# Kernel optimization log

Measured on AMD Instinct MI355X. Metric: run time of the kernel, lower is better.

## Reference

```python
import jax, jax.numpy as jnp
import numpy as np

N_NODES = 100000
N_EDGES = 3200000
IN_F, HID, OUT_F = 128, 3, 4


def setup_inputs() -> dict:
    key = jax.random.key(0)
    k1, k2, k3, k4, k5, k6 = jax.random.split(key, 6)
    x = jax.random.normal(k1, (N_NODES, IN_F), dtype=jnp.float32)
    edge_index = jax.random.randint(k2, (2, N_EDGES), 0, N_NODES, dtype=jnp.int64)
    # GCNConv weight (glorot) + bias, Linear(3,4) weight + bias
    W = jax.random.normal(k3, (IN_F, HID), dtype=jnp.float32) * (1.0 / np.sqrt(IN_F))
    b = jnp.zeros((HID,), dtype=jnp.float32)
    Wout = jax.random.normal(k4, (HID, OUT_F), dtype=jnp.float32) * (1.0 / np.sqrt(HID))
    bout = jax.random.normal(k5, (OUT_F,), dtype=jnp.float32) * 0.01
    return {"x": x, "edge_index": edge_index, "W": W, "b": b, "Wout": Wout, "bout": bout}


def reference(x, edge_index, W, b, Wout, bout):
    N = x.shape[0]
    # add self loops (PyG GCNConv default: add_self_loops=True)
    loop = jnp.arange(N, dtype=edge_index.dtype)
    row = jnp.concatenate([edge_index[0], loop])  # source nodes
    col = jnp.concatenate([edge_index[1], loop])  # destination nodes
    # linear transform first (cheaper: 128 -> 3)
    xw = x @ W  # [N, 3]
    # symmetric degree normalization: deg computed on destination index
    deg = jax.ops.segment_sum(jnp.ones_like(col, dtype=x.dtype), col, num_segments=N)
    dinv = jnp.where(deg > 0, jax.lax.rsqrt(deg), 0.0)
    norm = dinv[row] * dinv[col]  # [E+N]
    # gather source features, scale, scatter-add to destinations
    msg = xw[row] * norm[:, None]  # [E+N, 3]
    agg = jax.ops.segment_sum(msg, col, num_segments=N)  # [N, 3]
    h = jax.nn.relu(agg + b)
    z = h @ Wout + bout
    return (h, z)
```

## Files before the change

### kernel.cpp

```cpp
#include <hip/hip_runtime.h>
#include <hip/hip_fp16.h>

#define N_NODES 100000
#define N_EDGES 3200000
#define IN_F    128
#define HID     3
#define OUT_F   4

#define BSHIFT  7
#define BSIZE   128
#define NBUCK   ((N_NODES + BSIZE - 1) / BSIZE)
#define NBLKA   512
#define EPB     ((N_EDGES + NBLKA - 1) / NBLKA)
#define NH      (NBUCK * NBLKA)

#define SCAN_ITEMS 16
#define SCAN_BLOCK 256
#define SCAN_PER_BLOCK (SCAN_ITEMS * SCAN_BLOCK)
#define NS1 ((NH + SCAN_PER_BLOCK - 1) / SCAN_PER_BLOCK)

#define NREP    4
#define RSTRIDE 392
#define CSTRIDE 136

typedef float f32x4 __attribute__((ext_vector_type(4)));


__global__ void xw_kernel(const float* __restrict__ x,
                          const float* __restrict__ W,
                          float* __restrict__ xw) {
    int wave = threadIdx.x >> 6;
    int lane = threadIdx.x & 63;
    int half = lane >> 5;
    int l    = lane & 31;
    int node = blockIdx.x * 8 + wave * 2 + half;
    if (node >= N_NODES) return;

    f32x4 xv = __builtin_nontemporal_load(
        reinterpret_cast<const f32x4*>(x + (size_t)node * IN_F + l * 4));
    const float* w = W + l * 4 * HID;
    float s0 = xv.x * w[0] + xv.y * w[3] + xv.z * w[6] + xv.w * w[9];
    float s1 = xv.x * w[1] + xv.y * w[4] + xv.z * w[7] + xv.w * w[10];
    float s2 = xv.x * w[2] + xv.y * w[5] + xv.z * w[8] + xv.w * w[11];
    #pragma unroll
    for (int off = 16; off > 0; off >>= 1) {
        s0 += __shfl_down(s0, off, 32);
        s1 += __shfl_down(s1, off, 32);
        s2 += __shfl_down(s2, off, 32);
    }
    if (l == 0) {
        xw[node * 3 + 0] = s0;
        xw[node * 3 + 1] = s1;
        xw[node * 3 + 2] = s2;
    }
}

__global__ __launch_bounds__(512) void histA_kernel(const int* __restrict__ col,
                                                    int* __restrict__ histG) {
    __shared__ int hist[NBUCK];
    int tid = threadIdx.x, blk = blockIdx.x;
    for (int i = tid; i < NBUCK; i += 512) hist[i] = 0;
    __syncthreads();
    int start = blk * EPB, end = min(start + EPB, N_EDGES);
    for (int e = start + tid; e < end; e += 512)
        atomicAdd(&hist[__builtin_nontemporal_load(&col[e]) >> BSHIFT], 1);
    __syncthreads();
    for (int i = tid; i < NBUCK; i += 512)
        histG[i * NBLKA + blk] = hist[i];
}

__global__ void scan1_kernel(int* __restrict__ data, int* __restrict__ bsum) {
    __shared__ int s[SCAN_BLOCK];
    int tid = threadIdx.x;
    int base = blockIdx.x * SCAN_PER_BLOCK + tid * SCAN_ITEMS;
    int v[SCAN_ITEMS];
    int tsum = 0;
    #pragma unroll
    for (int j = 0; j < SCAN_ITEMS; ++j) {
        v[j] = (base + j < NH) ? data[base + j] : 0;
        tsum += v[j];
    }
    s[tid] = tsum;
    __syncthreads();
    for (int off = 1; off < SCAN_BLOCK; off <<= 1) {
        int t = (tid >= off) ? s[tid - off] : 0;
        __syncthreads();
        s[tid] += t;
        __syncthreads();
    }
    int run = s[tid] - tsum;
    #pragma unroll
    for (int j = 0; j < SCAN_ITEMS; ++j) {
        int t = v[j];
        if (base + j < NH) data[base + j] = run;
        run += t;
    }
    if (tid == SCAN_BLOCK - 1) bsum[blockIdx.x] = s[SCAN_BLOCK - 1];
}

__global__ void scan2_kernel(int* __restrict__ bsum) {
    __shared__ int s[SCAN_BLOCK];
    int tid = threadIdx.x;
    int v = (tid < NS1) ? bsum[tid] : 0;
    s[tid] = v;
    __syncthreads();
    for (int off = 1; off < SCAN_BLOCK; off <<= 1) {
        int t = (tid >= off) ? s[tid - off] : 0;
        __syncthreads();
        s[tid] += t;
        __syncthreads();
    }
    if (tid < NS1) bsum[tid] = s[tid] - v;
}

__global__ void scan3_kernel(int* __restrict__ data, const int* __restrict__ bsum) {
    int i = blockIdx.x * blockDim.x + threadIdx.x;
    if (i < NH) data[i] += bsum[i / SCAN_PER_BLOCK];
}

__global__ __launch_bounds__(512) void fillB_kernel(const int* __restrict__ row,
                                                    const int* __restrict__ col,
                                                    const int* __restrict__ histG,
                                                    int* __restrict__ packed) {
    __shared__ int offs[NBUCK];
    int tid = threadIdx.x, blk = blockIdx.x;
    for (int i = tid; i < NBUCK; i += 512) offs[i] = histG[i * NBLKA + blk];
    __syncthreads();
    int start = blk * EPB, end = min(start + EPB, N_EDGES);
    for (int e = start + tid; e < end; e += 512) {
        int c = __builtin_nontemporal_load(&col[e]);
        int r = __builtin_nontemporal_load(&row[e]);
        int b = c >> BSHIFT;
        int pos = atomicAdd(&offs[b], 1);
        packed[pos] = (r << BSHIFT) | (c & (BSIZE - 1));
    }
}

__global__ __launch_bounds__(512, 8) void degC_kernel(const int* __restrict__ histG,
                                                      const int* __restrict__ packed,
                                                      const float* __restrict__ xw,
                                                      uint2* __restrict__ tab) {
    __shared__ int cnt[NREP * CSTRIDE];
    int tid = threadIdx.x, b = blockIdx.x;
    int rep = tid & (NREP - 1);
    for (int i = tid; i < NREP * CSTRIDE; i += 512) cnt[i] = 0;
    __syncthreads();
    int start = histG[b * NBLKA];
    int end   = (b + 1 < NBUCK) ? histG[(b + 1) * NBLKA] : N_EDGES;
    int len   = end - start;
    int nfull = len & ~(4 * 512 - 1);
    for (int off = tid; off < nfull; off += 2048) {
        int p0 = __builtin_nontemporal_load(&packed[start + off]);
        int p1 = __builtin_nontemporal_load(&packed[start + off + 512]);
        int p2 = __builtin_nontemporal_load(&packed[start + off + 1024]);
        int p3 = __builtin_nontemporal_load(&packed[start + off + 1536]);
        atomicAdd(&cnt[rep * CSTRIDE + (p0 & (BSIZE - 1))], 1);
        atomicAdd(&cnt[rep * CSTRIDE + (p1 & (BSIZE - 1))], 1);
        atomicAdd(&cnt[rep * CSTRIDE + (p2 & (BSIZE - 1))], 1);
        atomicAdd(&cnt[rep * CSTRIDE + (p3 & (BSIZE - 1))], 1);
    }
    for (int off = nfull + tid; off < len; off += 512)
        atomicAdd(&cnt[rep * CSTRIDE + (__builtin_nontemporal_load(&packed[start + off]) & (BSIZE - 1))], 1);
    __syncthreads();
    if (tid < BSIZE) {
        int node = b * BSIZE + tid;
        if (node < N_NODES) {
            int c = cnt[0 * CSTRIDE + tid] + cnt[1 * CSTRIDE + tid]
                  + cnt[2 * CSTRIDE + tid] + cnt[3 * CSTRIDE + tid];
            float d = rsqrtf((float)(c + 1));
            __half2 lo = __floats2half2_rn(xw[node * 3 + 0] * d, xw[node * 3 + 1] * d);
            __half2 hi = __floats2half2_rn(xw[node * 3 + 2] * d, d);
            uint2 u;
            u.x = *reinterpret_cast<unsigned int*>(&lo);
            u.y = *reinterpret_cast<unsigned int*>(&hi);
            tab[node] = u;
        }
    }
}

__device__ inline void unpack4(uint2 u, float& a, float& b, float& c, float& d) {
    __half2 lo = *reinterpret_cast<__half2*>(&u.x);
    __half2 hi = *reinterpret_cast<__half2*>(&u.y);
    float2 f0 = __half22float2(lo);
    float2 f1 = __half22float2(hi);
    a = f0.x; b = f0.y; c = f1.x; d = f1.y;
}

__global__ __launch_bounds__(512, 8) void aggC_kernel(const int* __restrict__ histG,
                                                      const int* __restrict__ packed,
                                                      const uint2* __restrict__ tab,
                                                      const float* __restrict__ bb,
                                                      const float* __restrict__ Wout,
                                                      const float* __restrict__ bout,
                                                      float* __restrict__ out) {
    __shared__ float acc[NREP * RSTRIDE];
    int tid = threadIdx.x, b = blockIdx.x;
    int rep = tid & (NREP - 1);
    float* myacc = acc + rep * RSTRIDE;
    for (int i = tid; i < NREP * RSTRIDE; i += 512) acc[i] = 0.f;
    __syncthreads();
    int start = histG[b * NBLKA];
    int end   = (b + 1 < NBUCK) ? histG[(b + 1) * NBLKA] : N_EDGES;
    int len   = end - start;
    int nfull = len & ~(4 * 512 - 1);
    for (int off = tid; off < nfull; off += 2048) {
        int p0 = __builtin_nontemporal_load(&packed[start + off]);
        int p1 = __builtin_nontemporal_load(&packed[start + off + 512]);
        int p2 = __builtin_nontemporal_load(&packed[start + off + 1024]);
        int p3 = __builtin_nontemporal_load(&packed[start + off + 1536]);
        uint2 u0 = tab[p0 >> BSHIFT];
        uint2 u1 = tab[p1 >> BSHIFT];
        uint2 u2 = tab[p2 >> BSHIFT];
        uint2 u3 = tab[p3 >> BSHIFT];
        float a0, b0, c0, d0, a1, b1, c1, d1, a2, b2, c2, d2, a3, b3, c3, d3;
        unpack4(u0, a0, b0, c0, d0);
        unpack4(u1, a1, b1, c1, d1);
        unpack4(u2, a2, b2, c2, d2);
        unpack4(u3, a3, b3, c3, d3);
        int i0 = (p0 & (BSIZE - 1)) * 3, i1 = (p1 & (BSIZE - 1)) * 3;
        int i2 = (p2 & (BSIZE - 1)) * 3, i3 = (p3 & (BSIZE - 1)) * 3;
        atomicAdd(&myacc[i0 + 0], a0); atomicAdd(&myacc[i0 + 1], b0); atomicAdd(&myacc[i0 + 2], c0);
        atomicAdd(&myacc[i1 + 0], a1); atomicAdd(&myacc[i1 + 1], b1); atomicAdd(&myacc[i1 + 2], c1);
        atomicAdd(&myacc[i2 + 0], a2); atomicAdd(&myacc[i2 + 1], b2); atomicAdd(&myacc[i2 + 2], c2);
        atomicAdd(&myacc[i3 + 0], a3); atomicAdd(&myacc[i3 + 1], b3); atomicAdd(&myacc[i3 + 2], c3);
    }
    for (int off = nfull + tid; off < len; off += 512) {
        int p = __builtin_nontemporal_load(&packed[start + off]);
        uint2 u = tab[p >> BSHIFT];
        float a, bq, c, d;
        unpack4(u, a, bq, c, d);
        int i = (p & (BSIZE - 1)) * 3;
        atomicAdd(&myacc[i + 0], a);
        atomicAdd(&myacc[i + 1], bq);
        atomicAdd(&myacc[i + 2], c);
    }
    __syncthreads();
    if (tid < BSIZE) {
        int node = b * BSIZE + tid;
        if (node < N_NODES) {
            float sx, sy, sz, di;
            unpack4(tab[node], sx, sy, sz, di);
            float g0 = sx, g1 = sy, g2 = sz;
            #pragma unroll
            for (int rr = 0; rr < NREP; ++rr) {
                g0 += acc[rr * RSTRIDE + tid * 3 + 0];
                g1 += acc[rr * RSTRIDE + tid * 3 + 1];
                g2 += acc[rr * RSTRIDE + tid * 3 + 2];
            }
            float h0 = fmaxf(g0 * di + bb[0], 0.f);
            float h1 = fmaxf(g1 * di + bb[1], 0.f);
            float h2 = fmaxf(g2 * di + bb[2], 0.f);
            out[node * 3 + 0] = h0;
            out[node * 3 + 1] = h1;
            out[node * 3 + 2] = h2;
            float* z = out + (size_t)N_NODES * 3;
            #pragma unroll
            for (int k = 0; k < 4; ++k) {
                z[node * 4 + k] = bout[k] + h0 * Wout[0 * 4 + k]
                                          + h1 * Wout[1 * 4 + k]
                                          + h2 * Wout[2 * 4 + k];
            }
        }
    }
}

extern "C" void kernel_launch(void* const* d_in, const int* in_sizes, int n_in,
                              void* d_out, int out_size, void* d_ws, size_t ws_size,
                              hipStream_t stream) {
    const float* x    = (const float*)d_in[0];
    const int*   ei   = (const int*)d_in[1];
    const float* W    = (const float*)d_in[2];
    const float* b    = (const float*)d_in[3];
    const float* Wout = (const float*)d_in[4];
    const float* bout = (const float*)d_in[5];
    float* out = (float*)d_out;

    char* wsb = (char*)d_ws;
    int*   histG  = (int*)(wsb);
    int*   packed = (int*)(wsb + (size_t)NH * 4);
    float* xw     = (float*)(wsb + (size_t)NH * 4 + (size_t)N_EDGES * 4);
    uint2* tab    = (uint2*)((char*)xw + (size_t)N_NODES * 3 * 4);
    int*   bsum   = (int*)((char*)tab + (size_t)N_NODES * 8);

    const int* row = ei;
    const int* col = ei + N_EDGES;

    const int B = 256;
    int gridX  = (N_NODES + 7) / 8;
    int gridS3 = (NH + B - 1) / B;

    xw_kernel<<<gridX, B, 0, stream>>>(x, W, xw);
    histA_kernel<<<NBLKA, 512, 0, stream>>>(col, histG);
    scan1_kernel<<<NS1, SCAN_BLOCK, 0, stream>>>(histG, bsum);
    scan2_kernel<<<1, SCAN_BLOCK, 0, stream>>>(bsum);
    scan3_kernel<<<gridS3, B, 0, stream>>>(histG, bsum);
    fillB_kernel<<<NBLKA, 512, 0, stream>>>(row, col, histG, packed);
    degC_kernel<<<NBUCK, 512, 0, stream>>>(histG, packed, xw, tab);
    aggC_kernel<<<NBUCK, 512, 0, stream>>>(histG, packed, tab, b, Wout, bout, out);
}
```

Before: 267.5 us.

## Two-level bucket sort edges so source features gather from LDS tiles

New measurement: 282.4 us. 1.06x slower.

```diff
diff --git a/kernel.cpp b/kernel.cpp
--- a/kernel.cpp
+++ b/kernel.cpp
@@ -7,24 +7,29 @@
 #define HID     3
 #define OUT_F   4
 
-#define BSHIFT  7
-#define BSIZE   128
-#define NBUCK   ((N_NODES + BSIZE - 1) / BSIZE)
-#define NBLKA   512
+#define DSH     10
+#define DTILE   1024
+#define DMASK   1023
+#define NSTRIPE 98
+#define SSH     12
+#define STILE   4096
+#define SMASK   4095
+#define NTILE   25
+#define NCH     16
+
+#define NBLKA   1024
+#define THRA    256
 #define EPB     ((N_EDGES + NBLKA - 1) / NBLKA)
-#define NH      (NBUCK * NBLKA)
+#define N1      (NSTRIPE * NBLKA)
 
 #define SCAN_ITEMS 16
 #define SCAN_BLOCK 256
 #define SCAN_PER_BLOCK (SCAN_ITEMS * SCAN_BLOCK)
-#define NS1 ((NH + SCAN_PER_BLOCK - 1) / SCAN_PER_BLOCK)
-
-#define NREP    4
-#define RSTRIDE 392
-#define CSTRIDE 136
+#define NS1 ((N1 + SCAN_PER_BLOCK - 1) / SCAN_PER_BLOCK)
+
+#define PSZ (NSTRIPE * DTILE * 3)
 
 typedef float f32x4 __attribute__((ext_vector_type(4)));
-
 
 __global__ void xw_kernel(const float* __restrict__ x,
                           const float* __restrict__ W,
@@ -35,7 +40,6 @@
     int l    = lane & 31;
     int node = blockIdx.x * 8 + wave * 2 + half;
     if (node >= N_NODES) return;
-
     f32x4 xv = __builtin_nontemporal_load(
         reinterpret_cast<const f32x4*>(x + (size_t)node * IN_F + l * 4));
     const float* w = W + l * 4 * HID;
@@ -55,18 +59,23 @@
     }
 }
 
-__global__ __launch_bounds__(512) void histA_kernel(const int* __restrict__ col,
-                                                    int* __restrict__ histG) {
-    __shared__ int hist[NBUCK];
+__global__ __launch_bounds__(THRA) void hist1_kernel(const int* __restrict__ col,
+                                                     int* __restrict__ histG) {
+    __shared__ int hist[8 * NSTRIPE];
     int tid = threadIdx.x, blk = blockIdx.x;
-    for (int i = tid; i < NBUCK; i += 512) hist[i] = 0;
+    for (int i = tid; i < 8 * NSTRIPE; i += THRA) hist[i] = 0;
     __syncthreads();
     int start = blk * EPB, end = min(start + EPB, N_EDGES);
-    for (int e = start + tid; e < end; e += 512)
-        atomicAdd(&hist[__builtin_nontemporal_load(&col[e]) >> BSHIFT], 1);
-    __syncthreads();
-    for (int i = tid; i < NBUCK; i += 512)
-        histG[i * NBLKA + blk] = hist[i];
+    for (int e = start + tid; e < end; e += THRA)
+        atomicAdd(&hist[(tid & 7) * NSTRIPE +
+                        (__builtin_nontemporal_load(&col[e]) >> DSH)], 1);
+    __syncthreads();
+    for (int s = tid; s < NSTRIPE; s += THRA) {
+        int v = 0;
+        #pragma unroll
+        for (int r = 0; r < 8; ++r) v += hist[r * NSTRIPE + s];
+        histG[s * NBLKA + blk] = v;
+    }
 }
 
 __global__ void scan1_kernel(int* __restrict__ data, int* __restrict__ bsum) {
@@ -77,7 +86,7 @@
     int tsum = 0;
     #pragma unroll
     for (int j = 0; j < SCAN_ITEMS; ++j) {
-        v[j] = (base + j < NH) ? data[base + j] : 0;
+        v[j] = (base + j < N1) ? data[base + j] : 0;
         tsum += v[j];
     }
     s[tid] = tsum;
@@ -92,7 +101,7 @@
     #pragma unroll
     for (int j = 0; j < SCAN_ITEMS; ++j) {
         int t = v[j];
-        if (base + j < NH) data[base + j] = run;
+        if (base + j < N1) data[base + j] = run;
         run += t;
     }
     if (tid == SCAN_BLOCK - 1) bsum[blockIdx.x] = s[SCAN_BLOCK - 1];
@@ -115,59 +124,67 @@
 
 __global__ void scan3_kernel(int* __restrict__ data, const int* __restrict__ bsum) {
     int i = blockIdx.x * blockDim.x + threadIdx.x;
-    if (i < NH) data[i] += bsum[i / SCAN_PER_BLOCK];
-}
-
-__global__ __launch_bounds__(512) void fillB_kernel(const int* __restrict__ row,
-                                                    const int* __restrict__ col,
-                                                    const int* __restrict__ histG,
-                                                    int* __restrict__ packed) {
-    __shared__ int offs[NBUCK];
+    if (i < N1) data[i] += bsum[i / SCAN_PER_BLOCK];
+}
+
+__global__ __launch_bounds__(THRA) void fill1_kernel(const int* __restrict__ row,
+                                                     const int* __restrict__ col,
+                                                     const int* __restrict__ histG,
+                                                     int* __restrict__ packed1) {
+    __shared__ int offs[NSTRIPE];
     int tid = threadIdx.x, blk = blockIdx.x;
-    for (int i = tid; i < NBUCK; i += 512) offs[i] = histG[i * NBLKA + blk];
+    for (int i = tid; i < NSTRIPE; i += THRA) offs[i] = histG[i * NBLKA + blk];
     __syncthreads();
     int start = blk * EPB, end = min(start + EPB, N_EDGES);
-    for (int e = start + tid; e < end; e += 512) {
+    for (int e = start + tid; e < end; e += THRA) {
         int c = __builtin_nontemporal_load(&col[e]);
         int r = __builtin_nontemporal_load(&row[e]);
-        int b = c >> BSHIFT;
-        int pos = atomicAdd(&offs[b], 1);
-        packed[pos] = (r << BSHIFT) | (c & (BSIZE - 1));
-    }
-}
-
-__global__ __launch_bounds__(512, 8) void degC_kernel(const int* __restrict__ histG,
-                                                      const int* __restrict__ packed,
-                                                      const float* __restrict__ xw,
-                                                      uint2* __restrict__ tab) {
-    __shared__ int cnt[NREP * CSTRIDE];
-    int tid = threadIdx.x, b = blockIdx.x;
-    int rep = tid & (NREP - 1);
-    for (int i = tid; i < NREP * CSTRIDE; i += 512) cnt[i] = 0;
-    __syncthreads();
-    int start = histG[b * NBLKA];
-    int end   = (b + 1 < NBUCK) ? histG[(b + 1) * NBLKA] : N_EDGES;
-    int len   = end - start;
-    int nfull = len & ~(4 * 512 - 1);
-    for (int off = tid; off < nfull; off += 2048) {
-        int p0 = __builtin_nontemporal_load(&packed[start + off]);
-        int p1 = __builtin_nontemporal_load(&packed[start + off + 512]);
-        int p2 = __builtin_nontemporal_load(&packed[start + off + 1024]);
-        int p3 = __builtin_nontemporal_load(&packed[start + off + 1536]);
-        atomicAdd(&cnt[rep * CSTRIDE + (p0 & (BSIZE - 1))], 1);
-        atomicAdd(&cnt[rep * CSTRIDE + (p1 & (BSIZE - 1))], 1);
-        atomicAdd(&cnt[rep * CSTRIDE + (p2 & (BSIZE - 1))], 1);
-        atomicAdd(&cnt[rep * CSTRIDE + (p3 & (BSIZE - 1))], 1);
-    }
-    for (int off = nfull + tid; off < len; off += 512)
-        atomicAdd(&cnt[rep * CSTRIDE + (__builtin_nontemporal_load(&packed[start + off]) & (BSIZE - 1))], 1);
-    __syncthreads();
-    if (tid < BSIZE) {
-        int node = b * BSIZE + tid;
+        int s = c >> DSH;
+        int pos = atomicAdd(&offs[s], 1);
+        packed1[pos] = (r << DSH) | (c & DMASK);
+    }
+}
+
+__global__ __launch_bounds__(1024) void prep_kernel(const int* __restrict__ histG,
+                                                    const int* __restrict__ packed1,
+                                                    const float* __restrict__ xw,
+                                                    uint2* __restrict__ tab,
+                                                    int* __restrict__ off2) {
+    __shared__ int cnt[DTILE];
+    __shared__ int h2[NTILE * NCH];
+    __shared__ int sc[NTILE * NCH];
+    int tid = threadIdx.x, s = blockIdx.x;
+    for (int i = tid; i < DTILE; i += 1024) cnt[i] = 0;
+    if (tid < NTILE * NCH) h2[tid] = 0;
+    __syncthreads();
+    int seg0 = histG[s * NBLKA];
+    int seg1 = (s + 1 < NSTRIPE) ? histG[(s + 1) * NBLKA] : N_EDGES;
+    int seglen = seg1 - seg0;
+    int chsz = (seglen + NCH - 1) / NCH;
+    if (chsz == 0) chsz = 1;
+    for (int i = seg0 + tid; i < seg1; i += 1024) {
+        int p = __builtin_nontemporal_load(&packed1[i]);
+        atomicAdd(&cnt[p & DMASK], 1);
+        int t = p >> (DSH + SSH);
+        int ch = (i - seg0) / chsz;
+        atomicAdd(&h2[t * NCH + ch], 1);
+    }
+    __syncthreads();
+    if (tid < NTILE * NCH) sc[tid] = h2[tid];
+    __syncthreads();
+    for (int off = 1; off < NTILE * NCH; off <<= 1) {
+        int v = 0;
+        if (tid < NTILE * NCH && tid >= off) v = sc[tid - off];
+        __syncthreads();
+        if (tid < NTILE * NCH) sc[tid] += v;
+        __syncthreads();
+    }
+    if (tid < NTILE * NCH)
+        off2[s * (NTILE * NCH) + tid] = seg0 + sc[tid] - h2[tid];
+    if (tid < DTILE) {
+        int node = s * DTILE + tid;
         if (node < N_NODES) {
-            int c = cnt[0 * CSTRIDE + tid] + cnt[1 * CSTRIDE + tid]
-                  + cnt[2 * CSTRIDE + tid] + cnt[3 * CSTRIDE + tid];
-            float d = rsqrtf((float)(c + 1));
+            float d = rsqrtf((float)(cnt[tid] + 1));
             __half2 lo = __floats2half2_rn(xw[node * 3 + 0] * d, xw[node * 3 + 1] * d);
             __half2 hi = __floats2half2_rn(xw[node * 3 + 2] * d, d);
             uint2 u;
@@ -178,91 +195,109 @@
     }
 }
 
-__device__ inline void unpack4(uint2 u, float& a, float& b, float& c, float& d) {
+__global__ __launch_bounds__(256) void fill2_kernel(const int* __restrict__ histG,
+                                                    const int* __restrict__ off2,
+                                                    const int* __restrict__ packed1,
+                                                    int* __restrict__ packed2) {
+    __shared__ int offs[NTILE];
+    int tid = threadIdx.x;
+    int s = blockIdx.x >> 4;
+    int c = blockIdx.x & (NCH - 1);
+    int seg0 = histG[s * NBLKA];
+    int seg1 = (s + 1 < NSTRIPE) ? histG[(s + 1) * NBLKA] : N_EDGES;
+    int seglen = seg1 - seg0;
+    int chsz = (seglen + NCH - 1) / NCH;
+    if (chsz == 0) chsz = 1;
+    if (tid < NTILE) offs[tid] = off2[s * (NTILE * NCH) + tid * NCH + c];
+    __syncthreads();
+    int lo = seg0 + c * chsz;
+    int hi = min(lo + chsz, seg1);
+    for (int i = lo + tid; i < hi; i += 256) {
+        int p = __builtin_nontemporal_load(&packed1[i]);
+        int t = p >> (DSH + SSH);
+        int pos = atomicAdd(&offs[t], 1);
+        packed2[pos] = (((p >> DSH) & SMASK) << DSH) | (p & DMASK);
+    }
+}
+
+__global__ __launch_bounds__(512) void aggF_kernel(const int* __restrict__ histG,
+                                                   const int* __restrict__ off2,
+                                                   const int* __restrict__ packed2,
+                                                   const uint2* __restrict__ tab,
+                                                   float* __restrict__ partial) {
+    __shared__ uint2 stab[STILE];
+    __shared__ float acc[DTILE * 3];
+    const int tq[5] = {0, 7, 13, 19, 25};
+    int tid = threadIdx.x;
+    int s = blockIdx.x >> 2;
+    int q = blockIdx.x & 3;
+    for (int i = tid; i < DTILE * 3; i += 512) acc[i] = 0.f;
+    int seg1 = (s + 1 < NSTRIPE) ? histG[(s + 1) * NBLKA] : N_EDGES;
+    for (int t = tq[q]; t < tq[q + 1]; ++t) {
+        __syncthreads();
+        for (int i = tid; i < STILE; i += 512) {
+            int g = t * STILE + i;
+            uint2 u = (g < N_NODES) ? tab[g] : make_uint2(0u, 0u);
+            stab[i] = u;
+        }
+        __syncthreads();
+        int b0 = off2[s * (NTILE * NCH) + t * NCH];
+        int b1 = (t + 1 < NTILE) ? off2[s * (NTILE * NCH) + (t + 1) * NCH] : seg1;
+        for (int i = b0 + tid; i < b1; i += 512) {
+            int p = __builtin_nontemporal_load(&packed2[i]);
+            uint2 v = stab[p >> DSH];
+            __half2 lo = *reinterpret_cast<__half2*>(&v.x);
+            __half2 hi = *reinterpret_cast<__half2*>(&v.y);
+            float2 f0 = __half22float2(lo);
+            float2 f1 = __half22float2(hi);
+            int a = (p & DMASK) * 3;
+            atomicAdd(&acc[a + 0], f0.x);
+            atomicAdd(&acc[a + 1], f0.y);
+            atomicAdd(&acc[a + 2], f1.x);
+        }
+    }
+    __syncthreads();
+    float* P = partial + (size_t)q * PSZ + (size_t)s * (DTILE * 3);
+    for (int i = tid; i < DTILE * 3; i += 512) P[i] = acc[i];
+}
+
+__global__ __launch_bounds__(256) void final_kernel(const float* __restrict__ partial,
+                                                    const uint2* __restrict__ tab,
+                                                    const float* __restrict__ bb,
+                                                    const float* __restrict__ Wout,
+                                                    const float* __restrict__ bout,
+                                                    float* __restrict__ out) {
+    int i = blockIdx.x * 256 + threadIdx.x;
+    if (i >= N_NODES) return;
+    uint2 u = tab[i];
     __half2 lo = *reinterpret_cast<__half2*>(&u.x);
     __half2 hi = *reinterpret_cast<__half2*>(&u.y);
     float2 f0 = __half22float2(lo);
     float2 f1 = __half22float2(hi);
-    a = f0.x; b = f0.y; c = f1.x; d = f1.y;
-}
-
-__global__ __launch_bounds__(512, 8) void aggC_kernel(const int* __restrict__ histG,
-                                                      const int* __restrict__ packed,
-                                                      const uint2* __restrict__ tab,
-                                                      const float* __restrict__ bb,
-                                                      const float* __restrict__ Wout,
-                                                      const float* __restrict__ bout,
-                                                      float* __restrict__ out) {
-    __shared__ float acc[NREP * RSTRIDE];
-    int tid = threadIdx.x, b = blockIdx.x;
-    int rep = tid & (NREP - 1);
-    float* myacc = acc + rep * RSTRIDE;
-    for (int i = tid; i < NREP * RSTRIDE; i += 512) acc[i] = 0.f;
-    __syncthreads();
-    int start = histG[b * NBLKA];
-    int end   = (b + 1 < NBUCK) ? histG[(b + 1) * NBLKA] : N_EDGES;
-    int len   = end - start;
-    int nfull = len & ~(4 * 512 - 1);
-    for (int off = tid; off < nfull; off += 2048) {
-        int p0 = __builtin_nontemporal_load(&packed[start + off]);
-        int p1 = __builtin_nontemporal_load(&packed[start + off + 512]);
-        int p2 = __builtin_nontemporal_load(&packed[start + off + 1024]);
-        int p3 = __builtin_nontemporal_load(&packed[start + off + 1536]);
-        uint2 u0 = tab[p0 >> BSHIFT];
-        uint2 u1 = tab[p1 >> BSHIFT];
-        uint2 u2 = tab[p2 >> BSHIFT];
-        uint2 u3 = tab[p3 >> BSHIFT];
-        float a0, b0, c0, d0, a1, b1, c1, d1, a2, b2, c2, d2, a3, b3, c3, d3;
-        unpack4(u0, a0, b0, c0, d0);
-        unpack4(u1, a1, b1, c1, d1);
-        unpack4(u2, a2, b2, c2, d2);
-        unpack4(u3, a3, b3, c3, d3);
-        int i0 = (p0 & (BSIZE - 1)) * 3, i1 = (p1 & (BSIZE - 1)) * 3;
-        int i2 = (p2 & (BSIZE - 1)) * 3, i3 = (p3 & (BSIZE - 1)) * 3;
-        atomicAdd(&myacc[i0 + 0], a0); atomicAdd(&myacc[i0 + 1], b0); atomicAdd(&myacc[i0 + 2], c0);
-        atomicAdd(&myacc[i1 + 0], a1); atomicAdd(&myacc[i1 + 1], b1); atomicAdd(&myacc[i1 + 2], c1);
-        atomicAdd(&myacc[i2 + 0], a2); atomicAdd(&myacc[i2 + 1], b2); atomicAdd(&myacc[i2 + 2], c2);
-        atomicAdd(&myacc[i3 + 0], a3); atomicAdd(&myacc[i3 + 1], b3); atomicAdd(&myacc[i3 + 2], c3);
-    }
-    for (int off = nfull + tid; off < len; off += 512) {
-        int p = __builtin_nontemporal_load(&packed[start + off]);
-        uint2 u = tab[p >> BSHIFT];
-        float a, bq, c, d;
-        unpack4(u, a, bq, c, d);
-        int i = (p & (BSIZE - 1)) * 3;
-        atomicAdd(&myacc[i + 0], a);
-        atomicAdd(&myacc[i + 1], bq);
-        atomicAdd(&myacc[i + 2], c);
-    }
-    __syncthreads();
-    if (tid < BSIZE) {
-        int node = b * BSIZE + tid;
-        if (node < N_NODES) {
-            float sx, sy, sz, di;
-            unpack4(tab[node], sx, sy, sz, di);
-            float g0 = sx, g1 = sy, g2 = sz;
-            #pragma unroll
-            for (int rr = 0; rr < NREP; ++rr) {
-                g0 += acc[rr * RSTRIDE + tid * 3 + 0];
-                g1 += acc[rr * RSTRIDE + tid * 3 + 1];
-                g2 += acc[rr * RSTRIDE + tid * 3 + 2];
-            }
-            float h0 = fmaxf(g0 * di + bb[0], 0.f);
-            float h1 = fmaxf(g1 * di + bb[1], 0.f);
-            float h2 = fmaxf(g2 * di + bb[2], 0.f);
-            out[node * 3 + 0] = h0;
-            out[node * 3 + 1] = h1;
-            out[node * 3 + 2] = h2;
-            float* z = out + (size_t)N_NODES * 3;
-            #pragma unroll
-            for (int k = 0; k < 4; ++k) {
-                z[node * 4 + k] = bout[k] + h0 * Wout[0 * 4 + k]
-                                          + h1 * Wout[1 * 4 + k]
-                                          + h2 * Wout[2 * 4 + k];
-            }
-        }
-    }
-}
+    float g0 = f0.x, g1 = f0.y, g2 = f1.x;
+    float di = f1.y;
+    #pragma unroll
+    for (int q = 0; q < 4; ++q) {
+        const float* P = partial + (size_t)q * PSZ + (size_t)i * 3;
+        g0 += P[0];
+        g1 += P[1];
+        g2 += P[2];
+    }
+    float h0 = fmaxf(g0 * di + bb[0], 0.f);
+    float h1 = fmaxf(g1 * di + bb[1], 0.f);
+    float h2 = fmaxf(g2 * di + bb[2], 0.f);
+    out[i * 3 + 0] = h0;
+    out[i * 3 + 1] = h1;
+    out[i * 3 + 2] = h2;
+    float* z = out + (size_t)N_NODES * 3;
+    #pragma unroll
+    for (int k = 0; k < 4; ++k) {
+        z[i * 4 + k] = bout[k] + h0 * Wout[0 * 4 + k] + h1 * Wout[1 * 4 + k]
+                                 + h2 * Wout[2 * 4 + k];
+    }
+}
+
+static inline size_t align256(size_t x) { return (x + 255) & ~(size_t)255; }
 
 extern "C" void kernel_launch(void* const* d_in, const int* in_sizes, int n_in,
                               void* d_out, int out_size, void* d_ws, size_t ws_size,
@@ -276,25 +311,27 @@
     float* out = (float*)d_out;
 
     char* wsb = (char*)d_ws;
-    int*   histG  = (int*)(wsb);
-    int*   packed = (int*)(wsb + (size_t)NH * 4);
-    float* xw     = (float*)(wsb + (size_t)NH * 4 + (size_t)N_EDGES * 4);
-    uint2* tab    = (uint2*)((char*)xw + (size_t)N_NODES * 3 * 4);
-    int*   bsum   = (int*)((char*)tab + (size_t)N_NODES * 8);
+    size_t off = 0;
+    int*   histG   = (int*)(wsb + off);  off = align256(off + (size_t)N1 * 4);
+    int*   packed1 = (int*)(wsb + off);  off = align256(off + (size_t)N_EDGES * 4);
+    int*   packed2 = (int*)(wsb + off);  off = align256(off + (size_t)N_EDGES * 4);
+    float* xw      = (float*)(wsb + off); off = align256(off + (size_t)N_NODES * 3 * 4);
+    uint2* tab     = (uint2*)(wsb + off); off = align256(off + (size_t)N_NODES * 8);
+    int*   off2    = (int*)(wsb + off);  off = align256(off + (size_t)NSTRIPE * NTILE * NCH * 4);
+    float* partial = (float*)(wsb + off); off = align256(off + (size_t)4 * PSZ * 4);
+    int*   bsum    = (int*)(wsb + off);  off = align256(off + (size_t)NS1 * 4);
 
     const int* row = ei;
     const int* col = ei + N_EDGES;
 
-    const int B = 256;
-    int gridX  = (N_NODES + 7) / 8;
-    int gridS3 = (NH + B - 1) / B;
-
-    xw_kernel<<<gridX, B, 0, stream>>>(x, W, xw);
-    histA_kernel<<<NBLKA, 512, 0, stream>>>(col, histG);
+    xw_kernel<<<(N_NODES + 7) / 8, 256, 0, stream>>>(x, W, xw);
+    hist1_kernel<<<NBLKA, THRA, 0, stream>>>(col, histG);
     scan1_kernel<<<NS1, SCAN_BLOCK, 0, stream>>>(histG, bsum);
     scan2_kernel<<<1, SCAN_BLOCK, 0, stream>>>(bsum);
-    scan3_kernel<<<gridS3, B, 0, stream>>>(histG, bsum);
-    fillB_kernel<<<NBLKA, 512, 0, stream>>>(row, col, histG, packed);
-    degC_kernel<<<NBUCK, 512, 0, stream>>>(histG, packed, xw, tab);
-    aggC_kernel<<<NBUCK, 512, 0, stream>>>(histG, packed, tab, b, Wout, bout, out);
-}
+    scan3_kernel<<<(N1 + 255) / 256, 256, 0, stream>>>(histG, bsum);
+    fill1_kernel<<<NBLKA, THRA, 0, stream>>>(row, col, histG, packed1);
+    prep_kernel<<<NSTRIPE, 1024, 0, stream>>>(histG, packed1, xw, tab, off2);
+    fill2_kernel<<<NSTRIPE * NCH, 256, 0, stream>>>(histG, off2, packed1, packed2);
+    aggF_kernel<<<NSTRIPE * 4, 512, 0, stream>>>(histG, off2, packed2, tab, partial);
+    final_kernel<<<(N_NODES + 255) / 256, 256, 0, stream>>>(partial, tab, b, Wout, bout, out);
+}
```
